# Performance work log

Measured on AMD Instinct MI355X. Metric: run time of the kernel, lower is better.

Reference implementation:

```python
import jax, jax.numpy as jnp
import numpy as np
import math

HEADS = 8

def setup_inputs() -> dict:
    key = jax.random.key(0)
    k1, k2 = jax.random.split(key)
    B, C, H, W = 8, 512, 32, 32
    x = jax.random.normal(k1, (B, C, H, W), dtype=jnp.float32)
    # weight-norm 1x1 conv params: v ~ N(0, 0.05), g initialized to ||v|| (torch weight_norm default)
    proj_v = jax.random.normal(k2, (3 * C, C), dtype=jnp.float32) * 0.05
    proj_g = jnp.linalg.norm(proj_v, axis=1)
    proj_b = jnp.zeros((3 * C,), dtype=jnp.float32)
    return {"x": x, "proj_v": proj_v, "proj_g": proj_g, "proj_b": proj_b}

def reference(x, proj_v, proj_g, proj_b):
    B, C, H, W = x.shape
    heads = HEADS
    dim = C // heads
    N = H * W
    # weight-normalized 1x1 conv: w = g * v / ||v|| per output channel
    w = proj_g[:, None] * proj_v / jnp.linalg.norm(proj_v, axis=1, keepdims=True)
    c = jnp.einsum('oc,bchw->bohw', w, x) + proj_b[None, :, None, None]
    c = c.reshape(B, 3, heads, dim, N)
    q, k, v = c[:, 0], c[:, 1], c[:, 2]  # each (B, heads, dim, N)
    scale = 1.0 / math.sqrt(dim)
    attn = jnp.einsum('bhdq,bhdk->bhqk', q, k) * scale  # (B, heads, N, N)
    attn = jax.nn.softmax(attn, axis=-1)
    out = jnp.einsum('bhdk,bhqk->bhdq', v, attn)  # (B, heads, dim, N)
    return x + out.reshape(B, C, H, W)
```

## Files before the change

kernel.cpp:

```cpp
#include <hip/hip_runtime.h>

typedef _Float16 f16;
typedef _Float16 f16x2 __attribute__((ext_vector_type(2)));
typedef _Float16 f16x4 __attribute__((ext_vector_type(4)));
typedef _Float16 f16x8 __attribute__((ext_vector_type(8)));
typedef float f32x4 __attribute__((ext_vector_type(4)));
typedef float f32x16 __attribute__((ext_vector_type(16)));
typedef unsigned int u32;
typedef unsigned int u32x4 __attribute__((ext_vector_type(4)));

__device__ inline f32x16 mfma32(f16x8 a, f16x8 b, f32x16 c) {
    return __builtin_amdgcn_mfma_f32_32x32x16_f16(a, b, c, 0, 0, 0);
}

__device__ inline u32 pk2u(float a, float b) {
    return __builtin_bit_cast(u32, __builtin_amdgcn_cvt_pkrtz(a, b));
}

__device__ inline void st8(f16* p, f16x8 v) {
    *(f16x4*)p = __builtin_shufflevector(v, v, 0, 1, 2, 3);
    *(f16x4*)(p + 4) = __builtin_shufflevector(v, v, 4, 5, 6, 7);
}
__device__ inline f16x8 ld8(const f16* p) {
    f16x4 lo = *(const f16x4*)p;
    f16x4 hi = *(const f16x4*)(p + 4);
    return __builtin_shufflevector(lo, hi, 0, 1, 2, 3, 4, 5, 6, 7);
}

__global__ __launch_bounds__(256) void prep_k(const float* __restrict__ pv,
                                              const float* __restrict__ pg,
                                              f16* __restrict__ w,
                                              const float* __restrict__ x,
                                              f16* __restrict__ xT) {
    int bid = blockIdx.x;
    if (bid < 1536) {
        int o = bid;
        const float* row = pv + (size_t)o * 512;
        float s = 0.f;
        for (int c = threadIdx.x; c < 512; c += 256) { float t = row[c]; s += t * t; }
        for (int off = 32; off; off >>= 1) s += __shfl_down(s, off, 64);
        __shared__ float red[4];
        int lane = threadIdx.x & 63, wid = threadIdx.x >> 6;
        if (lane == 0) red[wid] = s;
        __syncthreads();
        float tot = red[0] + red[1] + red[2] + red[3];
        float scale = pg[o] * rsqrtf(tot);
        for (int c = threadIdx.x; c < 512; c += 256)
            w[(size_t)o * 512 + c] = (f16)(row[c] * scale);
    } else {
        int t2 = bid - 1536;
        int n0 = (t2 & 31) * 32, c0 = ((t2 >> 5) & 15) * 32, b = t2 >> 9;
        int tx = threadIdx.x & 31, ty = threadIdx.x >> 5;
        __shared__ float t[32][33];
        const float* xb = x + (size_t)b * 512 * 1024;
        for (int i = 0; i < 4; i++)
            t[ty + 8 * i][tx] = xb[(size_t)(c0 + ty + 8 * i) * 1024 + n0 + tx];
        __syncthreads();
        f16* xTb = xT + (size_t)b * 1024 * 512;
        for (int i = 0; i < 4; i++)
            xTb[(size_t)(n0 + ty + 8 * i) * 512 + c0 + tx] = (f16)t[tx][ty + 8 * i];
    }
}

__global__ __launch_bounds__(256) void qkv_gemm_k(const f16* __restrict__ w,
                                                  const f16* __restrict__ xT,
                                                  const float* __restrict__ pb,
                                                  f16* __restrict__ qk,
                                                  f16* __restrict__ v) {
    __shared__ f16 lA[128 * 64];
    __shared__ f16 lB[128 * 64];
    int b = blockIdx.z;
    int oBase = blockIdx.y * 128;
    int nBase = blockIdx.x * 128;
    const f16* xb = xT + (size_t)b * 1024 * 512;
    int tid = threadIdx.x, lane = tid & 63, warp = tid >> 6;
    int wy = warp >> 1, wx = warp & 1;
    int l31 = lane & 31, hi = lane >> 5;

    int srow = lane >> 3;
    int phys = lane & 7;
    int schunk = phys ^ srow;
    const f16* aS[4]; const f16* bS[4]; int ldsOff[4];
    for (int j = 0; j < 4; j++) {
        int rb = (warp * 4 + j) * 8;
        aS[j] = w  + (size_t)(oBase + rb + srow) * 512 + schunk * 8;
        bS[j] = xb + (size_t)(nBase + rb + srow) * 512 + schunk * 8;
        ldsOff[j] = (rb + srow) * 64 + phys * 8;
    }
    int phk[4];
    for (int ks = 0; ks < 4; ks++)
        phk[ks] = (((ks * 2 + hi) ^ (l31 & 7))) * 8;

    f16x8 rA[4], rB[4];
    for (int j = 0; j < 4; j++) {
        rA[j] = *(const f16x8*)aS[j];
        rB[j] = *(const f16x8*)bS[j];
    }

    f32x16 acc[2][2] = {};

    for (int i = 0; i < 8; i++) {
        __syncthreads();
        for (int j = 0; j < 4; j++) {
            *(f16x8*)&lA[ldsOff[j]] = rA[j];
            *(f16x8*)&lB[ldsOff[j]] = rB[j];
        }
        __syncthreads();
        if (i < 7) {
            int k0 = (i + 1) * 64;
            for (int j = 0; j < 4; j++) {
                rA[j] = *(const f16x8*)(aS[j] + k0);
                rB[j] = *(const f16x8*)(bS[j] + k0);
            }
        }
        for (int ks = 0; ks < 4; ks++) {
            f16x8 af[2], bf[2];
            for (int mi = 0; mi < 2; mi++)
                af[mi] = *(f16x8*)&lA[(wy * 64 + mi * 32 + l31) * 64 + phk[ks]];
            for (int ni = 0; ni < 2; ni++)
                bf[ni] = *(f16x8*)&lB[(wx * 64 + ni * 32 + l31) * 64 + phk[ks]];
            for (int mi = 0; mi < 2; mi++)
                for (int ni = 0; ni < 2; ni++)
                    acc[mi][ni] = mfma32(af[mi], bf[ni], acc[mi][ni]);
        }
    }

    int selB = oBase >> 9;
    for (int mi = 0; mi < 2; mi++) {
        for (int g = 0; g < 4; g++) {
            int oR = oBase + wy * 64 + mi * 32 + 8 * g + 4 * hi;
            int h = (oR >> 6) & 7, d0 = oR & 63;
            for (int ni = 0; ni < 2; ni++) {
                int n = nBase + wx * 64 + ni * 32 + l31;
                if (selB < 2) {
                    float sc = selB == 0 ? 0.125f : 1.0f;
                    f16x4 o4;
                    for (int r = 0; r < 4; r++)
                        o4[r] = (f16)((acc[mi][ni][g * 4 + r] + pb[oR + r]) * sc);
                    *(f16x4*)&qk[((((size_t)b * 2 + selB) * 8 + h) * 1024 + n) * 64 + d0] = o4;
                } else {
                    for (int r = 0; r < 4; r++) {
                        float val = acc[mi][ni][g * 4 + r] + pb[oR + r];
                        v[(((size_t)b * 8 + h) * 64 + d0 + r) * 1024 + n] = (f16)val;
                    }
                }
            }
        }
    }
}

#define ALDK 68
__global__ __launch_bounds__(256, 2) void attn_k(const f16* __restrict__ qk,
                                                 const f16* __restrict__ vg,
                                                 const float* __restrict__ x,
                                                 float* __restrict__ out) {
    __shared__ __align__(16) f16 smem[2 * 64 * ALDK];
    f16* lK = smem;
    f16* lV = smem + 64 * ALDK;

    int bh = blockIdx.y;
    int b = bh >> 3, h = bh & 7;
    int qBase = blockIdx.x * 128;
    int tid = threadIdx.x, lane = tid & 63, warp = tid >> 6;
    int l31 = lane & 31, hi = lane >> 5;

    const f16* qbase = qk + (((size_t)b * 2 + 0) * 8 + h) * 1024 * 64;
    const f16* kbase = qk + (((size_t)b * 2 + 1) * 8 + h) * 1024 * 64;
    const f16* vbase = vg + ((size_t)b * 8 + h) * 64 * 1024;

    int q0 = qBase + warp * 32;
    f16x8 aq[4];
    for (int ks = 0; ks < 4; ks++)
        aq[ks] = *(const f16x8*)&qbase[(size_t)(q0 + l31) * 64 + ks * 16 + hi * 8];

    int sr0 = tid >> 3, sc0 = (tid & 7) * 8;
    int sr1 = sr0 + 32;

    f16x8 rK[2], rV[2];
    rK[0] = *(const f16x8*)&kbase[(size_t)sr0 * 64 + sc0];
    rK[1] = *(const f16x8*)&kbase[(size_t)sr1 * 64 + sc0];
    rV[0] = *(const f16x8*)&vbase[(size_t)sr0 * 1024 + sc0];
    rV[1] = *(const f16x8*)&vbase[(size_t)sr1 * 1024 + sc0];

    f32x16 accO[2] = {};
    float l_acc = 0.f;

    for (int kt = 0; kt < 16; kt++) {
        __syncthreads();
        st8(&lK[sr0 * ALDK + sc0], rK[0]);
        st8(&lK[sr1 * ALDK + sc0], rK[1]);
        st8(&lV[sr0 * ALDK + sc0], rV[0]);
        st8(&lV[sr1 * ALDK + sc0], rV[1]);
        __syncthreads();
        if (kt < 15) {
            const f16* kb = kbase + (size_t)(kt + 1) * 64 * 64;
            rK[0] = *(const f16x8*)&kb[(size_t)sr0 * 64 + sc0];
            rK[1] = *(const f16x8*)&kb[(size_t)sr1 * 64 + sc0];
            rV[0] = *(const f16x8*)&vbase[(size_t)sr0 * 1024 + (kt + 1) * 64 + sc0];
            rV[1] = *(const f16x8*)&vbase[(size_t)sr1 * 1024 + (kt + 1) * 64 + sc0];
        }

        u32 P0[2][4], P1[2][4];
        float rs = 0.f;
        for (int mt = 0; mt < 2; mt++) {
            f16x8 ak[4];
            for (int ks = 0; ks < 4; ks++)
                ak[ks] = ld8(&lK[(mt * 32 + l31) * ALDK + ks * 16 + hi * 8]);
            f32x16 stt = {};
            for (int ks = 0; ks < 4; ks++)
                stt = mfma32(ak[ks], aq[ks], stt);
            for (int g = 0; g < 4; g++) {
                float p0 = __expf(stt[g * 4 + 0]);
                float p1 = __expf(stt[g * 4 + 1]);
                float p2 = __expf(stt[g * 4 + 2]);
                float p3 = __expf(stt[g * 4 + 3]);
                rs += (p0 + p1) + (p2 + p3);
                P0[mt][g] = pk2u(p0, p1);
                P1[mt][g] = pk2u(p2, p3);
            }
        }
        l_acc += rs;

        f16x8 av[2][4];
        for (int dt = 0; dt < 2; dt++)
            for (int ks = 0; ks < 4; ks++)
                av[dt][ks] = ld8(&lV[(dt * 32 + l31) * ALDK + ks * 16 + hi * 8]);
        f16x8 bfrag[4];
        for (int ks = 0; ks < 4; ks++) {
            int mt = ks >> 1, ge = 2 * (ks & 1);
            u32 e00 = P0[mt][ge], e01 = P0[mt][ge + 1];
            u32 e10 = P1[mt][ge], e11 = P1[mt][ge + 1];
            u32 k0 = hi ? e01 : e00;
            u32 k1 = hi ? e11 : e10;
            u32 s0 = hi ? e00 : e01;
            u32 s1 = hi ? e10 : e11;
            u32 r0 = __shfl_xor(s0, 32, 64);
            u32 r1 = __shfl_xor(s1, 32, 64);
            u32 a0 = hi ? r0 : k0, a1 = hi ? r1 : k1;
            u32 b0 = hi ? k0 : r0, b1 = hi ? k1 : r1;
            u32x4 t = {a0, a1, b0, b1};
            bfrag[ks] = __builtin_bit_cast(f16x8, t);
        }
        for (int dt = 0; dt < 2; dt++)
            for (int ks = 0; ks < 4; ks++)
                accO[dt] = mfma32(av[dt][ks], bfrag[ks], accO[dt]);
    }

    float lt = l_acc + __shfl_xor(l_acc, 32, 64);
    float rl = 1.0f / lt;
    int q = q0 + l31;
    for (int dt = 0; dt < 2; dt++)
        for (int g = 0; g < 4; g++)
            for (int r = 0; r < 4; r++) {
                int d = dt * 32 + 8 * g + 4 * hi + r;
                size_t gi = ((size_t)b * 512 + h * 64 + d) * 1024 + q;
                out[gi] = x[gi] + accO[dt][g * 4 + r] * rl;
            }
}

extern "C" void kernel_launch(void* const* d_in, const int* in_sizes, int n_in,
                              void* d_out, int out_size, void* d_ws, size_t ws_size,
                              hipStream_t stream) {
    (void)in_sizes; (void)n_in; (void)out_size; (void)ws_size;
    const float* x  = (const float*)d_in[0];
    const float* pv = (const float*)d_in[1];
    const float* pg = (const float*)d_in[2];
    const float* pb = (const float*)d_in[3];
    float* out = (float*)d_out;

    char* ws = (char*)d_ws;
    f16* w   = (f16*)(ws);
    f16* xT  = (f16*)(ws + 1572864);
    f16* qk  = (f16*)(ws + 1572864 + 8388608);
    f16* v   = (f16*)(ws + 1572864 + 8388608 + 16777216);

    hipLaunchKernelGGL(prep_k,     dim3(5632),     dim3(256), 0, stream, pv, pg, w, x, xT);
    hipLaunchKernelGGL(qkv_gemm_k, dim3(8, 12, 8), dim3(256), 0, stream, w, xT, pb, qk, v);
    hipLaunchKernelGGL(attn_k,     dim3(8, 64),    dim3(256), 0, stream, qk, v, x, out);
}
```

Baseline: 128.5 us.

## Drop LDS staging; load MFMA fragments directly from global memory

Both the QKV GEMM and the attention kernel stop staging tiles through shared memory with register prefetch and barriers. Each wave now loads its MFMA operand fragments straight from global memory, relying on L1/L2 for reuse. This removes the LDS traffic and __syncthreads cost but loses the explicit double-buffered prefetch. In the attention kernel each of the four waves now re-reads the same K/V tile independently, which raises cache traffic and load latency on the critical path.

```diff
diff --git a/kernel.cpp b/kernel.cpp
--- a/kernel.cpp
+++ b/kernel.cpp
@@ -15,16 +15,6 @@
 
 __device__ inline u32 pk2u(float a, float b) {
     return __builtin_bit_cast(u32, __builtin_amdgcn_cvt_pkrtz(a, b));
-}
-
-__device__ inline void st8(f16* p, f16x8 v) {
-    *(f16x4*)p = __builtin_shufflevector(v, v, 0, 1, 2, 3);
-    *(f16x4*)(p + 4) = __builtin_shufflevector(v, v, 4, 5, 6, 7);
-}
-__device__ inline f16x8 ld8(const f16* p) {
-    f16x4 lo = *(const f16x4*)p;
-    f16x4 hi = *(const f16x4*)(p + 4);
-    return __builtin_shufflevector(lo, hi, 0, 1, 2, 3, 4, 5, 6, 7);
 }
 
 __global__ __launch_bounds__(256) void prep_k(const float* __restrict__ pv,
@@ -67,8 +57,6 @@
                                                   const float* __restrict__ pb,
                                                   f16* __restrict__ qk,
                                                   f16* __restrict__ v) {
-    __shared__ f16 lA[128 * 64];
-    __shared__ f16 lB[128 * 64];
     int b = blockIdx.z;
     int oBase = blockIdx.y * 128;
     int nBase = blockIdx.x * 128;
@@ -77,52 +65,22 @@
     int wy = warp >> 1, wx = warp & 1;
     int l31 = lane & 31, hi = lane >> 5;
 
-    int srow = lane >> 3;
-    int phys = lane & 7;
-    int schunk = phys ^ srow;
-    const f16* aS[4]; const f16* bS[4]; int ldsOff[4];
-    for (int j = 0; j < 4; j++) {
-        int rb = (warp * 4 + j) * 8;
-        aS[j] = w  + (size_t)(oBase + rb + srow) * 512 + schunk * 8;
-        bS[j] = xb + (size_t)(nBase + rb + srow) * 512 + schunk * 8;
-        ldsOff[j] = (rb + srow) * 64 + phys * 8;
-    }
-    int phk[4];
-    for (int ks = 0; ks < 4; ks++)
-        phk[ks] = (((ks * 2 + hi) ^ (l31 & 7))) * 8;
-
-    f16x8 rA[4], rB[4];
-    for (int j = 0; j < 4; j++) {
-        rA[j] = *(const f16x8*)aS[j];
-        rB[j] = *(const f16x8*)bS[j];
-    }
+    const f16* aRow[2];
+    const f16* bRow[2];
+    for (int mi = 0; mi < 2; mi++)
+        aRow[mi] = w  + (size_t)(oBase + wy * 64 + mi * 32 + l31) * 512 + hi * 8;
+    for (int ni = 0; ni < 2; ni++)
+        bRow[ni] = xb + (size_t)(nBase + wx * 64 + ni * 32 + l31) * 512 + hi * 8;
 
     f32x16 acc[2][2] = {};
 
-    for (int i = 0; i < 8; i++) {
-        __syncthreads();
-        for (int j = 0; j < 4; j++) {
-            *(f16x8*)&lA[ldsOff[j]] = rA[j];
-            *(f16x8*)&lB[ldsOff[j]] = rB[j];
-        }
-        __syncthreads();
-        if (i < 7) {
-            int k0 = (i + 1) * 64;
-            for (int j = 0; j < 4; j++) {
-                rA[j] = *(const f16x8*)(aS[j] + k0);
-                rB[j] = *(const f16x8*)(bS[j] + k0);
-            }
-        }
-        for (int ks = 0; ks < 4; ks++) {
-            f16x8 af[2], bf[2];
-            for (int mi = 0; mi < 2; mi++)
-                af[mi] = *(f16x8*)&lA[(wy * 64 + mi * 32 + l31) * 64 + phk[ks]];
+    for (int k = 0; k < 512; k += 16) {
+        f16x8 af[2], bf[2];
+        for (int mi = 0; mi < 2; mi++) af[mi] = *(const f16x8*)(aRow[mi] + k);
+        for (int ni = 0; ni < 2; ni++) bf[ni] = *(const f16x8*)(bRow[ni] + k);
+        for (int mi = 0; mi < 2; mi++)
             for (int ni = 0; ni < 2; ni++)
-                bf[ni] = *(f16x8*)&lB[(wx * 64 + ni * 32 + l31) * 64 + phk[ks]];
-            for (int mi = 0; mi < 2; mi++)
-                for (int ni = 0; ni < 2; ni++)
-                    acc[mi][ni] = mfma32(af[mi], bf[ni], acc[mi][ni]);
-        }
+                acc[mi][ni] = mfma32(af[mi], bf[ni], acc[mi][ni]);
     }
 
     int selB = oBase >> 9;
@@ -149,15 +107,10 @@
     }
 }
 
-#define ALDK 68
-__global__ __launch_bounds__(256, 2) void attn_k(const f16* __restrict__ qk,
-                                                 const f16* __restrict__ vg,
-                                                 const float* __restrict__ x,
-                                                 float* __restrict__ out) {
-    __shared__ __align__(16) f16 smem[2 * 64 * ALDK];
-    f16* lK = smem;
-    f16* lV = smem + 64 * ALDK;
-
+__global__ __launch_bounds__(256) void attn_k(const f16* __restrict__ qk,
+                                              const f16* __restrict__ vg,
+                                              const float* __restrict__ x,
+                                              float* __restrict__ out) {
     int bh = blockIdx.y;
     int b = bh >> 3, h = bh & 7;
     int qBase = blockIdx.x * 128;
@@ -173,42 +126,25 @@
     for (int ks = 0; ks < 4; ks++)
         aq[ks] = *(const f16x8*)&qbase[(size_t)(q0 + l31) * 64 + ks * 16 + hi * 8];
 
-    int sr0 = tid >> 3, sc0 = (tid & 7) * 8;
-    int sr1 = sr0 + 32;
-
-    f16x8 rK[2], rV[2];
-    rK[0] = *(const f16x8*)&kbase[(size_t)sr0 * 64 + sc0];
-    rK[1] = *(const f16x8*)&kbase[(size_t)sr1 * 64 + sc0];
-    rV[0] = *(const f16x8*)&vbase[(size_t)sr0 * 1024 + sc0];
-    rV[1] = *(const f16x8*)&vbase[(size_t)sr1 * 1024 + sc0];
+    const f16* kRow[2];
+    const f16* vRow[2];
+    for (int t = 0; t < 2; t++) {
+        kRow[t] = kbase + (size_t)(t * 32 + l31) * 64 + hi * 8;
+        vRow[t] = vbase + (size_t)(t * 32 + l31) * 1024 + hi * 8;
+    }
 
     f32x16 accO[2] = {};
     float l_acc = 0.f;
 
     for (int kt = 0; kt < 16; kt++) {
-        __syncthreads();
-        st8(&lK[sr0 * ALDK + sc0], rK[0]);
-        st8(&lK[sr1 * ALDK + sc0], rK[1]);
-        st8(&lV[sr0 * ALDK + sc0], rV[0]);
-        st8(&lV[sr1 * ALDK + sc0], rV[1]);
-        __syncthreads();
-        if (kt < 15) {
-            const f16* kb = kbase + (size_t)(kt + 1) * 64 * 64;
-            rK[0] = *(const f16x8*)&kb[(size_t)sr0 * 64 + sc0];
-            rK[1] = *(const f16x8*)&kb[(size_t)sr1 * 64 + sc0];
-            rV[0] = *(const f16x8*)&vbase[(size_t)sr0 * 1024 + (kt + 1) * 64 + sc0];
-            rV[1] = *(const f16x8*)&vbase[(size_t)sr1 * 1024 + (kt + 1) * 64 + sc0];
-        }
-
         u32 P0[2][4], P1[2][4];
         float rs = 0.f;
         for (int mt = 0; mt < 2; mt++) {
-            f16x8 ak[4];
-            for (int ks = 0; ks < 4; ks++)
-                ak[ks] = ld8(&lK[(mt * 32 + l31) * ALDK + ks * 16 + hi * 8]);
             f32x16 stt = {};
-            for (int ks = 0; ks < 4; ks++)
-                stt = mfma32(ak[ks], aq[ks], stt);
+            for (int ks = 0; ks < 4; ks++) {
+                f16x8 ak = *(const f16x8*)(kRow[mt] + (size_t)kt * 4096 + ks * 16);
+                stt = mfma32(ak, aq[ks], stt);
+            }
             for (int g = 0; g < 4; g++) {
                 float p0 = __expf(stt[g * 4 + 0]);
                 float p1 = __expf(stt[g * 4 + 1]);
@@ -221,10 +157,6 @@
         }
         l_acc += rs;
 
-        f16x8 av[2][4];
-        for (int dt = 0; dt < 2; dt++)
-            for (int ks = 0; ks < 4; ks++)
-                av[dt][ks] = ld8(&lV[(dt * 32 + l31) * ALDK + ks * 16 + hi * 8]);
         f16x8 bfrag[4];
         for (int ks = 0; ks < 4; ks++) {
             int mt = ks >> 1, ge = 2 * (ks & 1);
@@ -242,8 +174,10 @@
             bfrag[ks] = __builtin_bit_cast(f16x8, t);
         }
         for (int dt = 0; dt < 2; dt++)
-            for (int ks = 0; ks < 4; ks++)
-                accO[dt] = mfma32(av[dt][ks], bfrag[ks], accO[dt]);
+            for (int ks = 0; ks < 4; ks++) {
+                f16x8 av = *(const f16x8*)(vRow[dt] + kt * 64 + ks * 16);
+                accO[dt] = mfma32(av, bfrag[ks], accO[dt]);
+            }
     }
 
     float lt = l_acc + __shfl_xor(l_acc, 32, 64);
```

Measured after the change: 201.9 us. +57.2%, slower.
